# Kernel tuning notes

Hardware: AMD Instinct MI355X
Metric: run time of the kernel (lower is better)

The kernel has to match this reference:

```python
import jax, jax.numpy as jnp
import numpy as np

B, D, S = 4, 512, 2048
N_HEAD, SEQ_LEN = 4, 1024
SEQ_MAX = 1 + SEQ_LEN * 3 + 1 + SEQ_LEN + 2  # 4100
ACT, BEAM, MAX_TURN = 8, 10, 7
EPS = 1e-5


def setup_inputs() -> dict:
    key = jax.random.key(0)
    ks = jax.random.split(key, 18)
    sd = 1.0 / np.sqrt(D)
    s2d = 1.0 / np.sqrt(2 * D)
    f = jnp.float32
    return {
        "x": jax.random.normal(ks[0], (B, D, S), f),
        "weight": jax.random.normal(ks[1], (N_HEAD, SEQ_MAX, SEQ_MAX), f) * sd,
        "c2s_w1": jax.random.normal(ks[2], (D, D), f) * sd,
        "c2s_b1": jnp.zeros((D,), f),
        "c2s_w2": jax.random.normal(ks[3], (D, D), f) * sd,
        "c2s_b2": jnp.zeros((D,), f),
        "eg_w1": jax.random.normal(ks[4], (D, D), f) * sd,
        "eg_b1": jnp.zeros((D,), f),
        "eg_w2": jax.random.normal(ks[5], (D, D), f) * sd,
        "eg_b2": jnp.zeros((D,), f),
        "gna_w1": jax.random.normal(ks[6], (2 * D, D), f) * s2d,
        "gna_b1": jnp.zeros((D,), f),
        "gna_w2": jax.random.normal(ks[7], (D, ACT), f) * sd,
        "gna_b2": jnp.zeros((ACT,), f),
        "action": jax.random.normal(ks[8], (ACT, D), f),
        "ln_g": jnp.ones((D,), f),
        "ln_b": jnp.zeros((D,), f),
    }


def _mlp(h, w1, b1, w2, b2):
    return jax.nn.relu(h @ w1 + b1) @ w2 + b2


def _layernorm(h, g, b):
    mu = h.mean(-1, keepdims=True)
    hc = h - mu
    var = (hc * hc).mean(-1, keepdims=True)
    return hc * jax.lax.rsqrt(var + EPS) * g + b


def reference(x, weight, c2s_w1, c2s_b1, c2s_w2, c2s_b2,
              eg_w1, eg_b1, eg_w2, eg_b2,
              gna_w1, gna_b1, gna_w2, gna_b2,
              action, ln_g, ln_b):
    Bv, Dv, Sv = x.shape
    w0 = jnp.tril(weight[0, :Sv, :Sv])            # causal mixing over seq
    c = jax.nn.relu(x @ w0)                       # [B, D, S]
    ct = jnp.swapaxes(c, 1, 2)                    # [B, S, D]
    states = _mlp(ct, c2s_w1, c2s_b1, c2s_w2, c2s_b2)[:, :, None, :]  # [B,S,1,D]
    initial_states = states
    goal = _mlp(ct, eg_w1, eg_b1, eg_w2, eg_b2)[:, :, None, :]        # [B,S,1,D]
    states_prob = jnp.ones(states.shape[:3], x.dtype)                  # [B,S,1]
    history = jnp.zeros((Bv, Sv, BEAM, MAX_TURN), jnp.int32)

    for turn in range(MAX_TURN):  # beam width: 1 -> 8 -> 10 -> ... (shape changes, so python loop)
        beam_now = states.shape[2]
        goal_e = jnp.broadcast_to(goal, states.shape)
        action_prob = jax.nn.softmax(
            _mlp(jnp.concatenate([states, goal_e], axis=-1),
                 gna_w1, gna_b1, gna_w2, gna_b2), axis=-1)              # [B,S,beam,ACT]
        beam_next = min(beam_now * ACT, BEAM)
        combined = (states_prob[..., None] * action_prob).reshape(Bv, Sv, beam_now * ACT)
        states_prob, idx = jax.lax.top_k(combined, beam_next)           # [B,S,beam_next]
        beam_idx = idx // ACT
        act_idx = idx % ACT
        base = jnp.take_along_axis(states, beam_idx[..., None], axis=2)  # [B,S,beam_next,D]
        states = _layernorm(base + action[act_idx], ln_g, ln_b)
        history = jnp.take_along_axis(history, beam_idx[..., None], axis=2, mode="clip")
        history = history.at[:, :, :, turn].set(act_idx)

    best = jnp.argmax(states_prob, axis=-1)                              # [B,S]
    act0 = jnp.take_along_axis(history[:, :, :, 0], best[..., None], axis=2)  # [B,S,1]
    base = jnp.take_along_axis(
        initial_states,
        jnp.broadcast_to(best[:, :, None, None], (Bv, Sv, 1, Dv)),
        axis=2, mode="clip")                                             # beam dim is 1 -> clipped to 0
    final = _layernorm(base + action[act0], ln_g, ln_b)                  # [B,S,1,D]
    return jnp.swapaxes(final[:, :, 0, :], 1, 2)                          # [B,D,S]
```

## Files before the change

### kernel.cpp

```cpp
#include <hip/hip_runtime.h>

#define DD    512
#define SS    2048
#define NB    4
#define TOK   8192
#define SEQM  4100
#define NACT  8
#define NBEAM 10
#define LNEPS 1e-5f

typedef unsigned short u16;
typedef short short8_t __attribute__((ext_vector_type(8)));
typedef float f32x4 __attribute__((ext_vector_type(4)));

__device__ __forceinline__ unsigned fmono(float f) {
  unsigned u = __float_as_uint(f);
  return (u & 0x80000000u) ? ~u : (u | 0x80000000u);
}

__device__ __forceinline__ u16 f2bf(float f) {
  unsigned u = __float_as_uint(f);
  unsigned r = u + 0x7FFFu + ((u >> 16) & 1u);
  return (u16)(r >> 16);
}

__global__ __launch_bounds__(256) void k_gemm_tril(
    const float* __restrict__ X, const float* __restrict__ W,
    float* __restrict__ Ct)
{
  __shared__ float As[16][132];
  __shared__ float Bs[16][132];
  const int tid = threadIdx.x;
  const int m0 = blockIdx.x * 128;
  const int n0 = blockIdx.y * 128;
  const int tm = tid >> 4, tn = tid & 15;
  float acc[8][8];
#pragma unroll
  for (int i = 0; i < 8; i++)
#pragma unroll
    for (int j = 0; j < 8; j++) acc[i][j] = 0.f;

  for (int k0 = n0; k0 < SS; k0 += 16) {
#pragma unroll
    for (int i = 0; i < 2; i++) {
      int id = tid + 256 * i;
      int r = id >> 2;
      int c4 = (id & 3) << 2;
      float4 av = *(const float4*)(X + (size_t)(m0 + r) * SS + k0 + c4);
      As[c4 + 0][r] = av.x; As[c4 + 1][r] = av.y;
      As[c4 + 2][r] = av.z; As[c4 + 3][r] = av.w;
    }
#pragma unroll
    for (int i = 0; i < 2; i++) {
      int id = tid + 256 * i;
      int r = id >> 5;
      int c = (id & 31) << 2;
      int kg = k0 + r;
      float4 bv = *(const float4*)(W + (size_t)kg * SEQM + n0 + c);
      int nc = n0 + c;
      bv.x = (kg >= nc + 0) ? bv.x : 0.f;
      bv.y = (kg >= nc + 1) ? bv.y : 0.f;
      bv.z = (kg >= nc + 2) ? bv.z : 0.f;
      bv.w = (kg >= nc + 3) ? bv.w : 0.f;
      *(float4*)&Bs[r][c] = bv;
    }
    __syncthreads();
#pragma unroll
    for (int kk = 0; kk < 16; kk++) {
      float4 a0 = *(const float4*)&As[kk][tm * 8];
      float4 a1 = *(const float4*)&As[kk][tm * 8 + 4];
      float4 b0 = *(const float4*)&Bs[kk][tn * 8];
      float4 b1 = *(const float4*)&Bs[kk][tn * 8 + 4];
      float a[8] = {a0.x, a0.y, a0.z, a0.w, a1.x, a1.y, a1.z, a1.w};
      float b[8] = {b0.x, b0.y, b0.z, b0.w, b1.x, b1.y, b1.z, b1.w};
#pragma unroll
      for (int i = 0; i < 8; i++)
#pragma unroll
        for (int j = 0; j < 8; j++) acc[i][j] = fmaf(a[i], b[j], acc[i][j]);
    }
    __syncthreads();
  }
  const int bI = m0 >> 9;
  const int d0 = (m0 & 511) + tm * 8;
#pragma unroll
  for (int j = 0; j < 8; j++) {
    int s = n0 + tn * 8 + j;
    float4 v0, v1;
    v0.x = fmaxf(acc[0][j], 0.f); v0.y = fmaxf(acc[1][j], 0.f);
    v0.z = fmaxf(acc[2][j], 0.f); v0.w = fmaxf(acc[3][j], 0.f);
    v1.x = fmaxf(acc[4][j], 0.f); v1.y = fmaxf(acc[5][j], 0.f);
    v1.z = fmaxf(acc[6][j], 0.f); v1.w = fmaxf(acc[7][j], 0.f);
    float* dst = Ct + ((size_t)bI * SS + s) * DD + d0;
    *(float4*)dst = v0;
    *(float4*)(dst + 4) = v1;
  }
}

__global__ __launch_bounds__(256) void k_gemm512(
    const float* __restrict__ A, const float* __restrict__ W,
    const float* __restrict__ biasVec, const float* __restrict__ gpre,
    int rowsPerTok, int strideTok, float* __restrict__ C, int mode)
{
  __shared__ float As[16][132];
  __shared__ float Bs[16][132];
  const int tid = threadIdx.x;
  const int m0 = blockIdx.x * 128;
  const int n0 = blockIdx.y * 128;
  const int tm = tid >> 4, tn = tid & 15;

  const int c4 = (tid & 3) << 2;
  const int r0 = tid >> 2;
  const int r1 = r0 + 64;
  const int gm0 = m0 + r0, gm1 = m0 + r1;
  const int t0i = gm0 / rowsPerTok, t1i = gm1 / rowsPerTok;
  const float* arow0 =
      A + ((size_t)t0i * strideTok + (gm0 - t0i * rowsPerTok)) * DD;
  const float* arow1 =
      A + ((size_t)t1i * strideTok + (gm1 - t1i * rowsPerTok)) * DD;

  float acc[8][8];
#pragma unroll
  for (int i = 0; i < 8; i++)
#pragma unroll
    for (int j = 0; j < 8; j++) acc[i][j] = 0.f;

  for (int k0 = 0; k0 < DD; k0 += 16) {
    {
      float4 av = *(const float4*)(arow0 + k0 + c4);
      As[c4 + 0][r0] = av.x; As[c4 + 1][r0] = av.y;
      As[c4 + 2][r0] = av.z; As[c4 + 3][r0] = av.w;
      float4 av1 = *(const float4*)(arow1 + k0 + c4);
      As[c4 + 0][r1] = av1.x; As[c4 + 1][r1] = av1.y;
      As[c4 + 2][r1] = av1.z; As[c4 + 3][r1] = av1.w;
    }
#pragma unroll
    for (int i = 0; i < 2; i++) {
      int id = tid + 256 * i;
      int r = id >> 5;
      int c = (id & 31) << 2;
      *(float4*)&Bs[r][c] =
          *(const float4*)(W + (size_t)(k0 + r) * DD + n0 + c);
    }
    __syncthreads();
#pragma unroll
    for (int kk = 0; kk < 16; kk++) {
      float4 a0 = *(const float4*)&As[kk][tm * 8];
      float4 a1 = *(const float4*)&As[kk][tm * 8 + 4];
      float4 b0 = *(const float4*)&Bs[kk][tn * 8];
      float4 b1 = *(const float4*)&Bs[kk][tn * 8 + 4];
      float a[8] = {a0.x, a0.y, a0.z, a0.w, a1.x, a1.y, a1.z, a1.w};
      float b[8] = {b0.x, b0.y, b0.z, b0.w, b1.x, b1.y, b1.z, b1.w};
#pragma unroll
      for (int i = 0; i < 8; i++)
#pragma unroll
        for (int j = 0; j < 8; j++) acc[i][j] = fmaf(a[i], b[j], acc[i][j]);
    }
    __syncthreads();
  }
#pragma unroll
  for (int i = 0; i < 8; i++) {
    int m = m0 + tm * 8 + i;
    const float* brow = (mode == 2) ? (gpre + (size_t)(m / rowsPerTok) * DD)
                                    : biasVec;
#pragma unroll
    for (int j = 0; j < 8; j++) {
      int n = n0 + tn * 8 + j;
      float v = acc[i][j] + brow[n];
      if (mode >= 1) v = fmaxf(v, 0.f);
      acc[i][j] = v;
    }
    float* dst = C + (size_t)m * DD + n0 + tn * 8;
    float4 w0v, w1v;
    w0v.x = acc[i][0]; w0v.y = acc[i][1]; w0v.z = acc[i][2]; w0v.w = acc[i][3];
    w1v.x = acc[i][4]; w1v.y = acc[i][5]; w1v.z = acc[i][6]; w1v.w = acc[i][7];
    *(float4*)dst = w0v;
    *(float4*)(dst + 4) = w1v;
  }
}

__global__ __launch_bounds__(256) void k_wsplit(
    const float* __restrict__ W, u16* __restrict__ WTh, u16* __restrict__ WTl)
{
  const int n = blockIdx.x;
  const int k = blockIdx.y * 256 + threadIdx.x;
  float v = W[(size_t)k * DD + n];
  u16 h = f2bf(v);
  float hf = __uint_as_float((unsigned)h << 16);
  u16 l = f2bf(v - hf);
  WTh[(size_t)n * DD + k] = h;
  WTl[(size_t)n * DD + k] = l;
}

__global__ __launch_bounds__(256) void k_gemm_mfma(
    const float* __restrict__ A, const u16* __restrict__ WTh,
    const u16* __restrict__ WTl, const float* __restrict__ gpre,
    int rowsPerTok, int strideTok, float* __restrict__ C)
{
  __shared__ __attribute__((aligned(16))) u16 AsH[64][56];
  __shared__ __attribute__((aligned(16))) u16 AsL[64][56];
  __shared__ __attribute__((aligned(16))) u16 BsH[128][56];
  __shared__ __attribute__((aligned(16))) u16 BsL[128][56];
  const int tid = threadIdx.x;
  const int m0 = blockIdx.x * 64;
  const int n0 = blockIdx.y * 128;

  const int sar = tid >> 2;
  const int sak = (tid & 3) * 8;
  const int gm = m0 + sar;
  const int stok = gm / rowsPerTok;
  const float* arow =
      A + ((size_t)stok * strideTok + (gm - stok * rowsPerTok)) * DD;
  const int sbr = tid >> 1;
  const int sbk = (tid & 1) * 16;
  const u16* wth = WTh + (size_t)(n0 + sbr) * DD + sbk;
  const u16* wtl = WTl + (size_t)(n0 + sbr) * DD + sbk;

  const int lane = tid & 63;
  const int w = tid >> 6;
  const int wm = (w >> 1) * 32;
  const int wn = (w & 1) * 64;
  const int lrow = lane & 15;
  const int quad = lane >> 4;
  const int q8 = quad * 8;

  f32x4 acc[2][4];
  const f32x4 zz = {0.f, 0.f, 0.f, 0.f};
#pragma unroll
  for (int mt = 0; mt < 2; mt++)
#pragma unroll
    for (int nt = 0; nt < 4; nt++) acc[mt][nt] = zz;

  for (int k0 = 0; k0 < DD; k0 += 32) {
    __syncthreads();
    {
      float4 v0 = *(const float4*)(arow + k0 + sak);
      float4 v1 = *(const float4*)(arow + k0 + sak + 4);
      float vv[8] = {v0.x, v0.y, v0.z, v0.w, v1.x, v1.y, v1.z, v1.w};
      short8_t ph, pl;
#pragma unroll
      for (int j = 0; j < 8; j++) {
        u16 h = f2bf(vv[j]);
        float hf = __uint_as_float((unsigned)h << 16);
        ph[j] = (short)h;
        pl[j] = (short)f2bf(vv[j] - hf);
      }
      *(short8_t*)&AsH[sar][sak] = ph;
      *(short8_t*)&AsL[sar][sak] = pl;
    }
    {
      *(short8_t*)&BsH[sbr][sbk] = *(const short8_t*)(wth + k0);
      *(short8_t*)&BsH[sbr][sbk + 8] = *(const short8_t*)(wth + k0 + 8);
      *(short8_t*)&BsL[sbr][sbk] = *(const short8_t*)(wtl + k0);
      *(short8_t*)&BsL[sbr][sbk + 8] = *(const short8_t*)(wtl + k0 + 8);
    }
    __syncthreads();
    short8_t ah[2], al[2], bh[4], bl[4];
#pragma unroll
    for (int mt = 0; mt < 2; mt++) {
      ah[mt] = *(const short8_t*)&AsH[wm + mt * 16 + lrow][q8];
      al[mt] = *(const short8_t*)&AsL[wm + mt * 16 + lrow][q8];
    }
#pragma unroll
    for (int nt = 0; nt < 4; nt++) {
      bh[nt] = *(const short8_t*)&BsH[wn + nt * 16 + lrow][q8];
      bl[nt] = *(const short8_t*)&BsL[wn + nt * 16 + lrow][q8];
    }
#pragma unroll
    for (int mt = 0; mt < 2; mt++)
#pragma unroll
      for (int nt = 0; nt < 4; nt++) {
        acc[mt][nt] = __builtin_amdgcn_mfma_f32_16x16x32_bf16(
            al[mt], bh[nt], acc[mt][nt], 0, 0, 0);
        acc[mt][nt] = __builtin_amdgcn_mfma_f32_16x16x32_bf16(
            ah[mt], bl[nt], acc[mt][nt], 0, 0, 0);
        acc[mt][nt] = __builtin_amdgcn_mfma_f32_16x16x32_bf16(
            ah[mt], bh[nt], acc[mt][nt], 0, 0, 0);
      }
  }
#pragma unroll
  for (int mt = 0; mt < 2; mt++)
#pragma unroll
    for (int nt = 0; nt < 4; nt++) {
      const int n = n0 + wn + nt * 16 + lrow;
#pragma unroll
      for (int r = 0; r < 4; r++) {
        const int mc = m0 + wm + mt * 16 + quad * 4 + r;
        const int tk = mc / rowsPerTok;
        float v = acc[mt][nt][r] + gpre[(size_t)tk * DD + n];
        C[(size_t)mc * DD + n] = fmaxf(v, 0.f);
      }
    }
}

__global__ __launch_bounds__(256) void k_logits(
    const float* __restrict__ H1, const float* __restrict__ W2,
    const float* __restrict__ b2, float* __restrict__ L)
{
  __shared__ float sW2[NACT][DD];
  const int tid = threadIdx.x;
  for (int idx = tid; idx < NACT * DD; idx += 256) {
    int n = idx & (DD - 1);
    int a = idx >> 9;
    sW2[a][n] = W2[(size_t)n * NACT + a];
  }
  __syncthreads();
  const int wv = tid >> 6, lane = tid & 63;
  const int rbase = blockIdx.x * 16 + wv * 4;
  for (int rr = 0; rr < 4; rr++) {
    const int row = rbase + rr;
    const float* hrow = H1 + (size_t)row * DD;
    float accv[NACT];
#pragma unroll
    for (int a = 0; a < NACT; a++) accv[a] = 0.f;
#pragma unroll
    for (int i = 0; i < 8; i++) {
      float h = hrow[lane + 64 * i];
#pragma unroll
      for (int a = 0; a < NACT; a++) accv[a] += h * sW2[a][lane + 64 * i];
    }
#pragma unroll
    for (int a = 0; a < NACT; a++)
#pragma unroll
      for (int off = 32; off; off >>= 1) accv[a] += __shfl_xor(accv[a], off, 64);
    float outv = accv[0];
#pragma unroll
    for (int a = 1; a < NACT; a++)
      if (lane == a) outv = accv[a];
    if (lane < NACT) L[(size_t)row * NACT + lane] = outv + b2[lane];
  }
}

__global__ __launch_bounds__(256) void k_update(
    const float* __restrict__ logits, const float* __restrict__ oldStates,
    float* __restrict__ states, float* __restrict__ prob,
    int* __restrict__ act0, const float* __restrict__ action,
    const float* __restrict__ lng, const float* __restrict__ lnb,
    int turn, int beamNow, int beamNext, int strideOld, int writeStates)
{
  __shared__ float sComb[NBEAM * NACT];
  __shared__ float sProbOld[NBEAM];
  __shared__ int   sAct0Old[NBEAM];
  __shared__ float sOld[NBEAM][DD];
  __shared__ int   sBeamIdx[NBEAM];
  __shared__ int   sActIdx[NBEAM];
  __shared__ int   sNewAct0[NBEAM];
  __shared__ float sNewProb[NBEAM];
  __shared__ float sRed[4];
  __shared__ float sMu, sInv;
  const int tid = threadIdx.x;
  const int token = blockIdx.x;

  if (tid < beamNow) {
    sProbOld[tid] = (turn == 0) ? 1.0f : prob[token * NBEAM + tid];
    sAct0Old[tid] = (turn == 0) ? 0 : act0[token * NBEAM + tid];
  }
  __syncthreads();
  if (tid < beamNow) {
    const float* lg = logits + ((size_t)token * beamNow + tid) * NACT;
    float l[NACT];
    float mx = -1e30f;
#pragma unroll
    for (int a = 0; a < NACT; a++) { l[a] = lg[a]; mx = fmaxf(mx, l[a]); }
    float e[NACT];
    float sum = 0.f;
#pragma unroll
    for (int a = 0; a < NACT; a++) { e[a] = expf(l[a] - mx); sum += e[a]; }
    float p = sProbOld[tid];
#pragma unroll
    for (int a = 0; a < NACT; a++) sComb[tid * NACT + a] = p * (e[a] / sum);
  }
  __syncthreads();
  if (tid < 64) {
    const int n = beamNow * NACT;
    float v0 = (tid < n) ? sComb[tid] : -1.f;
    float v1 = (tid + 64 < n) ? sComb[tid + 64] : -1.f;
    for (int it = 0; it < beamNext; it++) {
      unsigned long long key0 =
          ((unsigned long long)fmono(v0) << 32) | (unsigned)(0xFFFFFFFFu - tid);
      unsigned long long key1 =
          ((unsigned long long)fmono(v1) << 32) |
          (unsigned)(0xFFFFFFFFu - (tid + 64));
      unsigned long long best = key0 > key1 ? key0 : key1;
#pragma unroll
      for (int off = 1; off < 64; off <<= 1) {
        unsigned long long o = __shfl_xor(best, off, 64);
        if (o > best) best = o;
      }
      int jw = (int)(0xFFFFFFFFu - (unsigned)(best & 0xFFFFFFFFu));
      if (tid == 0) {
        int bi = jw >> 3, ai = jw & 7;
        sBeamIdx[it] = bi;
        sActIdx[it] = ai;
        sNewProb[it] = sComb[jw];
        sNewAct0[it] = (turn == 0) ? ai : sAct0Old[bi];
      }
      if (jw == tid) v0 = -1.f;
      if (jw == tid + 64) v1 = -1.f;
    }
  }
  __syncthreads();
  if (tid < beamNext) {
    prob[token * NBEAM + tid] = sNewProb[tid];
    act0[token * NBEAM + tid] = sNewAct0[tid];
  }
  if (!writeStates) return;

  const float* oldBase = oldStates + (size_t)token * strideOld * DD;
  for (int idx = tid; idx < beamNow * DD; idx += 256)
    (&sOld[0][0])[idx] = oldBase[idx];
  __syncthreads();
  const int lane = tid & 63, wv = tid >> 6;
  for (int jb = 0; jb < beamNext; jb++) {
    int bi = sBeamIdx[jb], ai = sActIdx[jb];
    float v0 = sOld[bi][tid] + action[(size_t)ai * DD + tid];
    float v1 = sOld[bi][tid + 256] + action[(size_t)ai * DD + tid + 256];
    float s = v0 + v1;
#pragma unroll
    for (int off = 32; off; off >>= 1) s += __shfl_xor(s, off, 64);
    if (lane == 0) sRed[wv] = s;
    __syncthreads();
    if (tid == 0) sMu = (sRed[0] + sRed[1] + sRed[2] + sRed[3]) * (1.f / DD);
    __syncthreads();
    float mu = sMu;
    float h0 = v0 - mu, h1v = v1 - mu;
    float q = h0 * h0 + h1v * h1v;
#pragma unroll
    for (int off = 32; off; off >>= 1) q += __shfl_xor(q, off, 64);
    if (lane == 0) sRed[wv] = q;
    __syncthreads();
    if (tid == 0)
      sInv = 1.0f /
             sqrtf((sRed[0] + sRed[1] + sRed[2] + sRed[3]) * (1.f / DD) + LNEPS);
    __syncthreads();
    float inv = sInv;
    float* dst = states + ((size_t)token * NBEAM + jb) * DD;
    dst[tid] = h0 * inv * lng[tid] + lnb[tid];
    dst[tid + 256] = h1v * inv * lng[tid + 256] + lnb[tid + 256];
    __syncthreads();
  }
}

__global__ __launch_bounds__(256) void k_final_prep(
    const float* __restrict__ prob, const int* __restrict__ act0,
    const float* __restrict__ states0, const float* __restrict__ action,
    int* __restrict__ abest, float* __restrict__ muA, float* __restrict__ invA)
{
  __shared__ int sA;
  __shared__ float sRed[4];
  __shared__ float sMu;
  const int tid = threadIdx.x;
  const int token = blockIdx.x;
  if (tid == 0) {
    float best = prob[token * NBEAM];
    int bi = 0;
    for (int j = 1; j < NBEAM; j++) {
      float v = prob[token * NBEAM + j];
      if (v > best) { best = v; bi = j; }
    }
    sA = act0[token * NBEAM + bi];
  }
  __syncthreads();
  const int a = sA;
  const int lane = tid & 63, wv = tid >> 6;
  float v0 = states0[(size_t)token * DD + tid] + action[(size_t)a * DD + tid];
  float v1 = states0[(size_t)token * DD + tid + 256] +
             action[(size_t)a * DD + tid + 256];
  float s = v0 + v1;
#pragma unroll
  for (int off = 32; off; off >>= 1) s += __shfl_xor(s, off, 64);
  if (lane == 0) sRed[wv] = s;
  __syncthreads();
  if (tid == 0) sMu = (sRed[0] + sRed[1] + sRed[2] + sRed[3]) * (1.f / DD);
  __syncthreads();
  float mu = sMu;
  float h0 = v0 - mu, h1v = v1 - mu;
  float q = h0 * h0 + h1v * h1v;
#pragma unroll
  for (int off = 32; off; off >>= 1) q += __shfl_xor(q, off, 64);
  if (lane == 0) sRed[wv] = q;
  __syncthreads();
  if (tid == 0) {
    float var = (sRed[0] + sRed[1] + sRed[2] + sRed[3]) * (1.f / DD);
    muA[token] = mu;
    invA[token] = 1.0f / sqrtf(var + LNEPS);
    abest[token] = a;
  }
}

__global__ __launch_bounds__(256) void k_final_write(
    const float* __restrict__ states0, const float* __restrict__ action,
    const int* __restrict__ abest, const float* __restrict__ muA,
    const float* __restrict__ invA, const float* __restrict__ lng,
    const float* __restrict__ lnb, float* __restrict__ out)
{
  __shared__ float tile[32][65];
  const int t0 = blockIdx.x * 32;
  const int d0 = blockIdx.y * 64;
  const int tid = threadIdx.x;
  {
    int r = tid >> 3;
    int c = (tid & 7) * 8;
    int token = t0 + r;
    int a = abest[token];
    float mu = muA[token], inv = invA[token];
#pragma unroll
    for (int q = 0; q < 8; q++) {
      int d = d0 + c + q;
      float v = (states0[(size_t)token * DD + d] + action[(size_t)a * DD + d] -
                 mu) * inv * lng[d] + lnb[d];
      tile[r][c + q] = v;
    }
  }
  __syncthreads();
  {
    int dl = tid >> 2;
    int sc = (tid & 3) * 8;
    int b = t0 >> 11;
    int s0 = (t0 & 2047);
    float* dst = out + ((size_t)(b * DD + d0 + dl)) * SS + s0 + sc;
    float4 w0v, w1v;
    w0v.x = tile[sc + 0][dl]; w0v.y = tile[sc + 1][dl];
    w0v.z = tile[sc + 2][dl]; w0v.w = tile[sc + 3][dl];
    w1v.x = tile[sc + 4][dl]; w1v.y = tile[sc + 5][dl];
    w1v.z = tile[sc + 6][dl]; w1v.w = tile[sc + 7][dl];
    *(float4*)dst = w0v;
    *(float4*)(dst + 4) = w1v;
  }
}

extern "C" void kernel_launch(void* const* d_in, const int* in_sizes, int n_in,
                              void* d_out, int out_size, void* d_ws,
                              size_t ws_size, hipStream_t stream) {
  const float* x      = (const float*)d_in[0];
  const float* weight = (const float*)d_in[1];
  const float* c2s_w1 = (const float*)d_in[2];
  const float* c2s_b1 = (const float*)d_in[3];
  const float* c2s_w2 = (const float*)d_in[4];
  const float* c2s_b2 = (const float*)d_in[5];
  const float* eg_w1  = (const float*)d_in[6];
  const float* eg_b1  = (const float*)d_in[7];
  const float* eg_w2  = (const float*)d_in[8];
  const float* eg_b2  = (const float*)d_in[9];
  const float* gna_w1 = (const float*)d_in[10];
  const float* gna_b1 = (const float*)d_in[11];
  const float* gna_w2 = (const float*)d_in[12];
  const float* gna_b2 = (const float*)d_in[13];
  const float* action = (const float*)d_in[14];
  const float* ln_g   = (const float*)d_in[15];
  const float* ln_b   = (const float*)d_in[16];
  float* out = (float*)d_out;

  float* ws = (float*)d_ws;
  size_t o = 0;
  float* ct      = ws + o; o += (size_t)TOK * DD;
  float* htmp    = ws + o; o += (size_t)TOK * DD;
  float* states0 = ws + o; o += (size_t)TOK * DD;
  float* goal    = ws + o; o += (size_t)TOK * DD;
  float* gpre    = ws + o; o += (size_t)TOK * DD;
  float* states  = ws + o; o += (size_t)TOK * NBEAM * DD;
  float* h1      = ws + o; o += (size_t)TOK * NBEAM * DD;
  float* logitsB = ws + o; o += (size_t)TOK * NBEAM * NACT;
  float* probB   = ws + o; o += (size_t)TOK * NBEAM;
  int*   act0B   = (int*)(ws + o); o += (size_t)TOK * NBEAM;
  int*   abest   = (int*)(ws + o); o += TOK;
  float* muA     = ws + o; o += TOK;
  float* invA    = ws + o; o += TOK;
  u16*   WTh     = (u16*)(ws + o); o += (size_t)DD * DD / 2;
  u16*   WTl     = (u16*)(ws + o); o += (size_t)DD * DD / 2;

  dim3 blk(256);
  k_gemm_tril<<<dim3(16, 16), blk, 0, stream>>>(x, weight, ct);
  k_gemm512<<<dim3(TOK / 128, 4), blk, 0, stream>>>(ct, c2s_w1, c2s_b1, gpre, 1, 1, htmp, 1);
  k_gemm512<<<dim3(TOK / 128, 4), blk, 0, stream>>>(htmp, c2s_w2, c2s_b2, gpre, 1, 1, states0, 0);
  k_gemm512<<<dim3(TOK / 128, 4), blk, 0, stream>>>(ct, eg_w1, eg_b1, gpre, 1, 1, htmp, 1);
  k_gemm512<<<dim3(TOK / 128, 4), blk, 0, stream>>>(htmp, eg_w2, eg_b2, gpre, 1, 1, goal, 0);
  k_gemm512<<<dim3(TOK / 128, 4), blk, 0, stream>>>(goal, gna_w1 + (size_t)DD * DD, gna_b1, gpre, 1, 1, gpre, 0);

  k_wsplit<<<dim3(DD, 2), blk, 0, stream>>>(gna_w1, WTh, WTl);

  for (int turn = 0; turn < 7; turn++) {
    int beamNow  = (turn == 0) ? 1 : ((turn == 1) ? 8 : 10);
    int beamNext = (turn == 0) ? 8 : 10;
    int rows = TOK * beamNow;
    const float* cur = (turn == 0) ? states0 : states;
    int strideOld    = (turn == 0) ? 1 : NBEAM;
    k_gemm_mfma<<<dim3(rows / 64, 4), blk, 0, stream>>>(
        cur, WTh, WTl, gpre, beamNow, strideOld, h1);
    k_logits<<<dim3(rows / 16), blk, 0, stream>>>(h1, gna_w2, gna_b2, logitsB);
    k_update<<<dim3(TOK), blk, 0, stream>>>(logitsB, cur, states, probB, act0B,
                                            action, ln_g, ln_b, turn, beamNow,
                                            beamNext, strideOld,
                                            (turn < 6) ? 1 : 0);
  }

  k_final_prep<<<dim3(TOK), blk, 0, stream>>>(probB, act0B, states0, action, abest, muA, invA);
  k_final_write<<<dim3(TOK / 32, DD / 64), blk, 0, stream>>>(states0, action, abest, muA, invA, ln_g, ln_b, out);

  (void)in_sizes; (void)n_in; (void)out_size; (void)ws_size;
}
```

Before: 3.224 ms.

## Move causal mixing GEMM to split-bf16 MFMA and fuse logits into hidden GEMM

The causal tril GEMM moves from an fp32 FMA kernel to a split-bf16 (hi/lo, three-MFMA) matrix-core kernel. It uses 64x128 tiles and converts and masks operands on the fly while loading them into shared memory. The per-turn hidden-layer GEMM now applies the ReLU, stages the tile in shared memory and multiplies by the 8-column output weight there. It writes four partial logit sets per row, which the update kernel sums, so the large h1 buffer round trip and the separate logits kernel go away. The cost is more shared memory, an extra sync and split-bf16 precision on the tril GEMM.

```diff
diff --git a/kernel.cpp b/kernel.cpp
--- a/kernel.cpp
+++ b/kernel.cpp
@@ -24,76 +24,112 @@
   return (u16)(r >> 16);
 }
 
-__global__ __launch_bounds__(256) void k_gemm_tril(
+__global__ __launch_bounds__(256) void k_tril_mfma(
     const float* __restrict__ X, const float* __restrict__ W,
     float* __restrict__ Ct)
 {
-  __shared__ float As[16][132];
-  __shared__ float Bs[16][132];
+  __shared__ __attribute__((aligned(16))) u16 AsH[64][56];
+  __shared__ __attribute__((aligned(16))) u16 AsL[64][56];
+  __shared__ __attribute__((aligned(16))) u16 BsH[128][56];
+  __shared__ __attribute__((aligned(16))) u16 BsL[128][56];
   const int tid = threadIdx.x;
-  const int m0 = blockIdx.x * 128;
+  const int m0 = blockIdx.x * 64;
   const int n0 = blockIdx.y * 128;
-  const int tm = tid >> 4, tn = tid & 15;
-  float acc[8][8];
-#pragma unroll
-  for (int i = 0; i < 8; i++)
-#pragma unroll
-    for (int j = 0; j < 8; j++) acc[i][j] = 0.f;
-
-  for (int k0 = n0; k0 < SS; k0 += 16) {
-#pragma unroll
-    for (int i = 0; i < 2; i++) {
-      int id = tid + 256 * i;
-      int r = id >> 2;
-      int c4 = (id & 3) << 2;
-      float4 av = *(const float4*)(X + (size_t)(m0 + r) * SS + k0 + c4);
-      As[c4 + 0][r] = av.x; As[c4 + 1][r] = av.y;
-      As[c4 + 2][r] = av.z; As[c4 + 3][r] = av.w;
-    }
-#pragma unroll
-    for (int i = 0; i < 2; i++) {
-      int id = tid + 256 * i;
-      int r = id >> 5;
-      int c = (id & 31) << 2;
-      int kg = k0 + r;
-      float4 bv = *(const float4*)(W + (size_t)kg * SEQM + n0 + c);
-      int nc = n0 + c;
-      bv.x = (kg >= nc + 0) ? bv.x : 0.f;
-      bv.y = (kg >= nc + 1) ? bv.y : 0.f;
-      bv.z = (kg >= nc + 2) ? bv.z : 0.f;
-      bv.w = (kg >= nc + 3) ? bv.w : 0.f;
-      *(float4*)&Bs[r][c] = bv;
-    }
-    __syncthreads();
-#pragma unroll
-    for (int kk = 0; kk < 16; kk++) {
-      float4 a0 = *(const float4*)&As[kk][tm * 8];
-      float4 a1 = *(const float4*)&As[kk][tm * 8 + 4];
-      float4 b0 = *(const float4*)&Bs[kk][tn * 8];
-      float4 b1 = *(const float4*)&Bs[kk][tn * 8 + 4];
-      float a[8] = {a0.x, a0.y, a0.z, a0.w, a1.x, a1.y, a1.z, a1.w};
-      float b[8] = {b0.x, b0.y, b0.z, b0.w, b1.x, b1.y, b1.z, b1.w};
-#pragma unroll
-      for (int i = 0; i < 8; i++)
-#pragma unroll
-        for (int j = 0; j < 8; j++) acc[i][j] = fmaf(a[i], b[j], acc[i][j]);
-    }
-    __syncthreads();
+
+  const int sar = tid >> 2;
+  const int sak = (tid & 3) * 8;
+  const float* arow = X + (size_t)(m0 + sar) * SS;
+  const int sbk = tid >> 3;
+  const int sbc = (tid & 7) * 16;
+
+  const int lane = tid & 63;
+  const int w = tid >> 6;
+  const int wm = (w >> 1) * 32;
+  const int wn = (w & 1) * 64;
+  const int lrow = lane & 15;
+  const int quad = lane >> 4;
+  const int q8 = quad * 8;
+
+  f32x4 acc[2][4];
+  const f32x4 zz = {0.f, 0.f, 0.f, 0.f};
+#pragma unroll
+  for (int mt = 0; mt < 2; mt++)
+#pragma unroll
+    for (int nt = 0; nt < 4; nt++) acc[mt][nt] = zz;
+
+  for (int k0 = n0; k0 < SS; k0 += 32) {
+    __syncthreads();
+    {
+      float4 v0 = *(const float4*)(arow + k0 + sak);
+      float4 v1 = *(const float4*)(arow + k0 + sak + 4);
+      float vv[8] = {v0.x, v0.y, v0.z, v0.w, v1.x, v1.y, v1.z, v1.w};
+      short8_t ph, pl;
+#pragma unroll
+      for (int j = 0; j < 8; j++) {
+        u16 h = f2bf(vv[j]);
+        float hf = __uint_as_float((unsigned)h << 16);
+        ph[j] = (short)h;
+        pl[j] = (short)f2bf(vv[j] - hf);
+      }
+      *(short8_t*)&AsH[sar][sak] = ph;
+      *(short8_t*)&AsL[sar][sak] = pl;
+    }
+    {
+      int kg = k0 + sbk;
+      const float* wr = W + (size_t)kg * SEQM + n0 + sbc;
+#pragma unroll
+      for (int j4 = 0; j4 < 4; j4++) {
+        float4 v = *(const float4*)(wr + j4 * 4);
+        float vv[4] = {v.x, v.y, v.z, v.w};
+        int ncb = n0 + sbc + j4 * 4;
+#pragma unroll
+        for (int j = 0; j < 4; j++) {
+          float f = (kg >= ncb + j) ? vv[j] : 0.f;
+          u16 h = f2bf(f);
+          float hf = __uint_as_float((unsigned)h << 16);
+          BsH[sbc + j4 * 4 + j][sbk] = h;
+          BsL[sbc + j4 * 4 + j][sbk] = f2bf(f - hf);
+        }
+      }
+    }
+    __syncthreads();
+    short8_t ah[2], al[2], bh[4], bl[4];
+#pragma unroll
+    for (int mt = 0; mt < 2; mt++) {
+      ah[mt] = *(const short8_t*)&AsH[wm + mt * 16 + lrow][q8];
+      al[mt] = *(const short8_t*)&AsL[wm + mt * 16 + lrow][q8];
+    }
+#pragma unroll
+    for (int nt = 0; nt < 4; nt++) {
+      bh[nt] = *(const short8_t*)&BsH[wn + nt * 16 + lrow][q8];
+      bl[nt] = *(const short8_t*)&BsL[wn + nt * 16 + lrow][q8];
+    }
+#pragma unroll
+    for (int mt = 0; mt < 2; mt++)
+#pragma unroll
+      for (int nt = 0; nt < 4; nt++) {
+        acc[mt][nt] = __builtin_amdgcn_mfma_f32_16x16x32_bf16(
+            al[mt], bh[nt], acc[mt][nt], 0, 0, 0);
+        acc[mt][nt] = __builtin_amdgcn_mfma_f32_16x16x32_bf16(
+            ah[mt], bl[nt], acc[mt][nt], 0, 0, 0);
+        acc[mt][nt] = __builtin_amdgcn_mfma_f32_16x16x32_bf16(
+            ah[mt], bh[nt], acc[mt][nt], 0, 0, 0);
+      }
   }
   const int bI = m0 >> 9;
-  const int d0 = (m0 & 511) + tm * 8;
-#pragma unroll
-  for (int j = 0; j < 8; j++) {
-    int s = n0 + tn * 8 + j;
-    float4 v0, v1;
-    v0.x = fmaxf(acc[0][j], 0.f); v0.y = fmaxf(acc[1][j], 0.f);
-    v0.z = fmaxf(acc[2][j], 0.f); v0.w = fmaxf(acc[3][j], 0.f);
-    v1.x = fmaxf(acc[4][j], 0.f); v1.y = fmaxf(acc[5][j], 0.f);
-    v1.z = fmaxf(acc[6][j], 0.f); v1.w = fmaxf(acc[7][j], 0.f);
-    float* dst = Ct + ((size_t)bI * SS + s) * DD + d0;
-    *(float4*)dst = v0;
-    *(float4*)(dst + 4) = v1;
-  }
+#pragma unroll
+  for (int mt = 0; mt < 2; mt++)
+#pragma unroll
+    for (int nt = 0; nt < 4; nt++) {
+      int s = n0 + wn + nt * 16 + lrow;
+      int d0 = (m0 & 511) + wm + mt * 16 + quad * 4;
+      float4 v;
+      v.x = fmaxf(acc[mt][nt][0], 0.f);
+      v.y = fmaxf(acc[mt][nt][1], 0.f);
+      v.z = fmaxf(acc[mt][nt][2], 0.f);
+      v.w = fmaxf(acc[mt][nt][3], 0.f);
+      *(float4*)(Ct + ((size_t)bI * SS + s) * DD + d0) = v;
+    }
 }
 
 __global__ __launch_bounds__(256) void k_gemm512(
@@ -194,12 +230,17 @@
 __global__ __launch_bounds__(256) void k_gemm_mfma(
     const float* __restrict__ A, const u16* __restrict__ WTh,
     const u16* __restrict__ WTl, const float* __restrict__ gpre,
-    int rowsPerTok, int strideTok, float* __restrict__ C)
+    const float* __restrict__ W2, int rowsPerTok, int strideTok,
+    float* __restrict__ logitsPart)
 {
-  __shared__ __attribute__((aligned(16))) u16 AsH[64][56];
-  __shared__ __attribute__((aligned(16))) u16 AsL[64][56];
-  __shared__ __attribute__((aligned(16))) u16 BsH[128][56];
-  __shared__ __attribute__((aligned(16))) u16 BsL[128][56];
+  __shared__ __attribute__((aligned(16))) unsigned char smem[43008];
+  u16 (*AsH)[56] = (u16 (*)[56])(smem);
+  u16 (*AsL)[56] = (u16 (*)[56])(smem + 7168);
+  u16 (*BsH)[56] = (u16 (*)[56])(smem + 14336);
+  u16 (*BsL)[56] = (u16 (*)[56])(smem + 28672);
+  float (*hs)[132]   = (float (*)[132])(smem);
+  float (*sW2t)[132] = (float (*)[132])(smem + 33792);
+
   const int tid = threadIdx.x;
   const int m0 = blockIdx.x * 64;
   const int n0 = blockIdx.y * 128;
@@ -277,65 +318,58 @@
             ah[mt], bh[nt], acc[mt][nt], 0, 0, 0);
       }
   }
+  __syncthreads();
 #pragma unroll
   for (int mt = 0; mt < 2; mt++)
 #pragma unroll
     for (int nt = 0; nt < 4; nt++) {
-      const int n = n0 + wn + nt * 16 + lrow;
+      const int nl = wn + nt * 16 + lrow;
 #pragma unroll
       for (int r = 0; r < 4; r++) {
-        const int mc = m0 + wm + mt * 16 + quad * 4 + r;
-        const int tk = mc / rowsPerTok;
-        float v = acc[mt][nt][r] + gpre[(size_t)tk * DD + n];
-        C[(size_t)mc * DD + n] = fmaxf(v, 0.f);
-      }
-    }
-}
-
-__global__ __launch_bounds__(256) void k_logits(
-    const float* __restrict__ H1, const float* __restrict__ W2,
-    const float* __restrict__ b2, float* __restrict__ L)
-{
-  __shared__ float sW2[NACT][DD];
-  const int tid = threadIdx.x;
-  for (int idx = tid; idx < NACT * DD; idx += 256) {
-    int n = idx & (DD - 1);
-    int a = idx >> 9;
-    sW2[a][n] = W2[(size_t)n * NACT + a];
-  }
-  __syncthreads();
-  const int wv = tid >> 6, lane = tid & 63;
-  const int rbase = blockIdx.x * 16 + wv * 4;
-  for (int rr = 0; rr < 4; rr++) {
-    const int row = rbase + rr;
-    const float* hrow = H1 + (size_t)row * DD;
-    float accv[NACT];
-#pragma unroll
-    for (int a = 0; a < NACT; a++) accv[a] = 0.f;
-#pragma unroll
-    for (int i = 0; i < 8; i++) {
-      float h = hrow[lane + 64 * i];
-#pragma unroll
-      for (int a = 0; a < NACT; a++) accv[a] += h * sW2[a][lane + 64 * i];
-    }
-#pragma unroll
-    for (int a = 0; a < NACT; a++)
-#pragma unroll
-      for (int off = 32; off; off >>= 1) accv[a] += __shfl_xor(accv[a], off, 64);
-    float outv = accv[0];
-#pragma unroll
-    for (int a = 1; a < NACT; a++)
-      if (lane == a) outv = accv[a];
-    if (lane < NACT) L[(size_t)row * NACT + lane] = outv + b2[lane];
+        const int ml = wm + mt * 16 + quad * 4 + r;
+        const int tk = (m0 + ml) / rowsPerTok;
+        float v = acc[mt][nt][r] + gpre[(size_t)tk * DD + n0 + nl];
+        hs[ml][nl] = fmaxf(v, 0.f);
+      }
+    }
+  for (int idx = tid; idx < 128 * NACT; idx += 256)
+    sW2t[idx & 7][idx >> 3] = W2[(size_t)n0 * NACT + idx];
+  __syncthreads();
+  {
+    const int rowl = w * 16 + (lane >> 2);
+    const int cq = lane & 3;
+    float part[NACT];
+#pragma unroll
+    for (int a = 0; a < NACT; a++) part[a] = 0.f;
+    for (int i = 0; i < 32; i++) {
+      int c = cq + 4 * i;
+      float h = hs[rowl][c];
+#pragma unroll
+      for (int a = 0; a < NACT; a++) part[a] = fmaf(h, sW2t[a][c], part[a]);
+    }
+#pragma unroll
+    for (int a = 0; a < NACT; a++) {
+      part[a] += __shfl_xor(part[a], 1, 64);
+      part[a] += __shfl_xor(part[a], 2, 64);
+    }
+    if (cq == 0) {
+      float* dst = logitsPart + (size_t)(m0 + rowl) * 32 + blockIdx.y * 8;
+      float4 p0, p1;
+      p0.x = part[0]; p0.y = part[1]; p0.z = part[2]; p0.w = part[3];
+      p1.x = part[4]; p1.y = part[5]; p1.z = part[6]; p1.w = part[7];
+      *(float4*)dst = p0;
+      *(float4*)(dst + 4) = p1;
+    }
   }
 }
 
 __global__ __launch_bounds__(256) void k_update(
-    const float* __restrict__ logits, const float* __restrict__ oldStates,
-    float* __restrict__ states, float* __restrict__ prob,
-    int* __restrict__ act0, const float* __restrict__ action,
-    const float* __restrict__ lng, const float* __restrict__ lnb,
-    int turn, int beamNow, int beamNext, int strideOld, int writeStates)
+    const float* __restrict__ logitsPart, const float* __restrict__ b2,
+    const float* __restrict__ oldStates, float* __restrict__ states,
+    float* __restrict__ prob, int* __restrict__ act0,
+    const float* __restrict__ action, const float* __restrict__ lng,
+    const float* __restrict__ lnb, int turn, int beamNow, int beamNext,
+    int strideOld, int writeStates)
 {
   __shared__ float sComb[NBEAM * NACT];
   __shared__ float sProbOld[NBEAM];
@@ -356,11 +390,14 @@
   }
   __syncthreads();
   if (tid < beamNow) {
-    const float* lg = logits + ((size_t)token * beamNow + tid) * NACT;
+    const float* lp = logitsPart + (size_t)(token * beamNow + tid) * 32;
     float l[NACT];
     float mx = -1e30f;
 #pragma unroll
-    for (int a = 0; a < NACT; a++) { l[a] = lg[a]; mx = fmaxf(mx, l[a]); }
+    for (int a = 0; a < NACT; a++) {
+      l[a] = lp[a] + lp[8 + a] + lp[16 + a] + lp[24 + a] + b2[a];
+      mx = fmaxf(mx, l[a]);
+    }
     float e[NACT];
     float sum = 0.f;
 #pragma unroll
@@ -552,24 +589,23 @@
 
   float* ws = (float*)d_ws;
   size_t o = 0;
-  float* ct      = ws + o; o += (size_t)TOK * DD;
-  float* htmp    = ws + o; o += (size_t)TOK * DD;
-  float* states0 = ws + o; o += (size_t)TOK * DD;
-  float* goal    = ws + o; o += (size_t)TOK * DD;
-  float* gpre    = ws + o; o += (size_t)TOK * DD;
-  float* states  = ws + o; o += (size_t)TOK * NBEAM * DD;
-  float* h1      = ws + o; o += (size_t)TOK * NBEAM * DD;
-  float* logitsB = ws + o; o += (size_t)TOK * NBEAM * NACT;
-  float* probB   = ws + o; o += (size_t)TOK * NBEAM;
-  int*   act0B   = (int*)(ws + o); o += (size_t)TOK * NBEAM;
-  int*   abest   = (int*)(ws + o); o += TOK;
-  float* muA     = ws + o; o += TOK;
-  float* invA    = ws + o; o += TOK;
-  u16*   WTh     = (u16*)(ws + o); o += (size_t)DD * DD / 2;
-  u16*   WTl     = (u16*)(ws + o); o += (size_t)DD * DD / 2;
+  float* ct       = ws + o; o += (size_t)TOK * DD;
+  float* htmp     = ws + o; o += (size_t)TOK * DD;
+  float* states0  = ws + o; o += (size_t)TOK * DD;
+  float* goal     = ws + o; o += (size_t)TOK * DD;
+  float* gpre     = ws + o; o += (size_t)TOK * DD;
+  float* states   = ws + o; o += (size_t)TOK * NBEAM * DD;
+  float* logitsP  = ws + o; o += (size_t)TOK * NBEAM * 32;
+  float* probB    = ws + o; o += (size_t)TOK * NBEAM;
+  int*   act0B    = (int*)(ws + o); o += (size_t)TOK * NBEAM;
+  int*   abest    = (int*)(ws + o); o += TOK;
+  float* muA      = ws + o; o += TOK;
+  float* invA     = ws + o; o += TOK;
+  u16*   WTh      = (u16*)(ws + o); o += (size_t)DD * DD / 2;
+  u16*   WTl      = (u16*)(ws + o); o += (size_t)DD * DD / 2;
 
   dim3 blk(256);
-  k_gemm_tril<<<dim3(16, 16), blk, 0, stream>>>(x, weight, ct);
+  k_tril_mfma<<<dim3(2048 / 64, SS / 128), blk, 0, stream>>>(x, weight, ct);
   k_gemm512<<<dim3(TOK / 128, 4), blk, 0, stream>>>(ct, c2s_w1, c2s_b1, gpre, 1, 1, htmp, 1);
   k_gemm512<<<dim3(TOK / 128, 4), blk, 0, stream>>>(htmp, c2s_w2, c2s_b2, gpre, 1, 1, states0, 0);
   k_gemm512<<<dim3(TOK / 128, 4), blk, 0, stream>>>(ct, eg_w1, eg_b1, gpre, 1, 1, htmp, 1);
@@ -585,12 +621,10 @@
     const float* cur = (turn == 0) ? states0 : states;
     int strideOld    = (turn == 0) ? 1 : NBEAM;
     k_gemm_mfma<<<dim3(rows / 64, 4), blk, 0, stream>>>(
-        cur, WTh, WTl, gpre, beamNow, strideOld, h1);
-    k_logits<<<dim3(rows / 16), blk, 0, stream>>>(h1, gna_w2, gna_b2, logitsB);
-    k_update<<<dim3(TOK), blk, 0, stream>>>(logitsB, cur, states, probB, act0B,
-                                            action, ln_g, ln_b, turn, beamNow,
-                                            beamNext, strideOld,
-                                            (turn < 6) ? 1 : 0);
+        cur, WTh, WTl, gpre, gna_w2, beamNow, strideOld, logitsP);
+    k_update<<<dim3(TOK), blk, 0, stream>>>(
+        logitsP, gna_b2, cur, states, probB, act0B, action, ln_g, ln_b,
+        turn, beamNow, beamNext, strideOld, (turn < 6) ? 1 : 0);
   }
 
   k_final_prep<<<dim3(TOK), blk, 0, stream>>>(probB, act0B, states0, action, abest, muA, invA);
```

After: 2.730 ms. 1.18x faster.
